# Kernel tuning notes

Hardware: AMD Instinct MI355X
Metric: run time of the kernel (lower is better)

## Reference

```python
import jax, jax.numpy as jnp
import numpy as np

N = 50000
IN_C = 128
OUT_C = 64


def gcn_conv(x, edge_index, W, b):
    # PyG GCNConv: h = X W; add self-loops; symmetric norm D^-1/2 (A+I) D^-1/2; aggregate; + bias
    n = x.shape[0]
    h = x @ W  # [N, out]
    loop = jnp.arange(n, dtype=edge_index.dtype)
    row = jnp.concatenate([edge_index[0], loop])  # source
    col = jnp.concatenate([edge_index[1], loop])  # target
    deg = jax.ops.segment_sum(jnp.ones_like(col, dtype=h.dtype), col, num_segments=n)
    dinv = jnp.where(deg > 0, jax.lax.rsqrt(deg), 0.0)
    norm = dinv[row] * dinv[col]  # [E+N]
    msg = norm[:, None] * h[row]  # gather source features
    out = jax.ops.segment_sum(msg, col, num_segments=n)  # scatter to targets
    return out + b


def layer_norm(x, w, b, eps=1e-5):
    mu = jnp.mean(x, axis=-1, keepdims=True)
    var = jnp.mean((x - mu) ** 2, axis=-1, keepdims=True)
    return (x - mu) * jax.lax.rsqrt(var + eps) * w + b


def setup_inputs() -> dict:
    key = jax.random.key(0)
    ks = jax.random.split(key, 10)
    x = jax.random.normal(ks[0], (N, IN_C), dtype=jnp.float32)
    edge_index = jax.random.randint(ks[1], (2, 800000), 0, N, dtype=jnp.int64)
    s1 = 1.0 / np.sqrt(IN_C)
    s2 = 1.0 / np.sqrt(OUT_C)
    W1 = jax.random.uniform(ks[2], (IN_C, OUT_C), jnp.float32, -s1, s1)
    b1 = jnp.zeros((OUT_C,), jnp.float32)
    ln_w = jnp.ones((OUT_C,), jnp.float32)
    ln_b = jnp.zeros((OUT_C,), jnp.float32)
    W2 = jax.random.uniform(ks[3], (OUT_C, OUT_C), jnp.float32, -s2, s2)
    b2 = jnp.zeros((OUT_C,), jnp.float32)
    W3 = jax.random.uniform(ks[4], (OUT_C, 6), jnp.float32, -s2, s2)
    b3 = jax.random.uniform(ks[5], (6,), jnp.float32, -s2, s2)
    return {"x": x, "edge_index": edge_index, "W1": W1, "b1": b1,
            "ln_w": ln_w, "ln_b": ln_b, "W2": W2, "b2": b2, "W3": W3, "b3": b3}


def reference(x, edge_index, W1, b1, ln_w, ln_b, W2, b2, W3, b3):
    h = gcn_conv(x, edge_index, W1, b1)           # [N, 64]
    h = jax.nn.relu(layer_norm(h, ln_w, ln_b))    # [N, 64]
    out1 = gcn_conv(h, edge_index, W2, b2)        # [N, 64]
    out2 = jax.nn.sigmoid(h @ W3 + b3)            # [N, 6]
    return (out1, out2)
```

## Files before the change

### kernel.cpp

```cpp
#include <hip/hip_runtime.h>
#include <hip/hip_fp16.h>
#include <math.h>


#define ELLW 48

typedef _Float16 half8 __attribute__((ext_vector_type(8)));
typedef float f32x4 __attribute__((ext_vector_type(4)));

__global__ void k_setup(const float* __restrict__ W1, const float* __restrict__ W2,
                        const float* __restrict__ W3, _Float16* __restrict__ W1g,
                        _Float16* __restrict__ Bg, int* __restrict__ cnt, int n) {
    if (blockIdx.x >= 52) {
        int i = (blockIdx.x - 52) * 256 + threadIdx.x;
        if (i < n) cnt[i] = 0;
        return;
    }
    int idx = blockIdx.x * 256 + threadIdx.x;
    if (idx < 8192) {
        int j = idx & 7, L = (idx >> 3) & 63, s = (idx >> 9) & 3, t = idx >> 11;
        int k = s * 32 + (L >> 4) * 8 + j;
        int c = t * 16 + (L & 15);
        W1g[idx] = (_Float16)W1[k * 64 + c];
    } else if (idx < 8192 + 5120) {
        int i2 = idx - 8192;
        int j = i2 & 7, L = (i2 >> 3) & 63, s = (i2 >> 9) & 1, u = i2 >> 10;
        int k = s * 32 + (L >> 4) * 8 + j;
        int c = (L & 15);
        float v;
        if (u < 4) v = W2[k * 64 + u * 16 + c];
        else v = (c < 6) ? W3[k * 6 + c] : 0.f;
        Bg[i2] = (_Float16)v;
    }
}

__global__ __launch_bounds__(256) void k_scatter(
    const int* __restrict__ row, const int* __restrict__ col,
    int* __restrict__ cnt, int* __restrict__ ell, int E, int slice_sz) {
    int slice = blockIdx.x & 7;
    int lo = slice * slice_sz;
    int hi = lo + slice_sz;
    int nchunk = gridDim.x >> 3;
    int stride = nchunk * 256;
    int v0 = (blockIdx.x >> 3) * 256 + threadIdx.x;
    int nv = E >> 2;
    const int4* c4p = (const int4*)col;
    const int4* r4p = (const int4*)row;
    for (int v = v0; v < nv; v += stride) {
        int4 c4 = c4p[v];
        int4 r4 = r4p[v];
        if (c4.x >= lo && c4.x < hi) {
            int rk = atomicAdd(&cnt[c4.x], 1);
            if (rk < ELLW) ell[c4.x * ELLW + rk] = r4.x << 7;
        }
        if (c4.y >= lo && c4.y < hi) {
            int rk = atomicAdd(&cnt[c4.y], 1);
            if (rk < ELLW) ell[c4.y * ELLW + rk] = r4.y << 7;
        }
        if (c4.z >= lo && c4.z < hi) {
            int rk = atomicAdd(&cnt[c4.z], 1);
            if (rk < ELLW) ell[c4.z * ELLW + rk] = r4.z << 7;
        }
        if (c4.w >= lo && c4.w < hi) {
            int rk = atomicAdd(&cnt[c4.w], 1);
            if (rk < ELLW) ell[c4.w * ELLW + rk] = r4.w << 7;
        }
    }
    if ((blockIdx.x >> 3) == 0) {
        for (int e = (nv << 2) + threadIdx.x; e < E; e += 256) {
            int c = col[e];
            if (c >= lo && c < hi) {
                int rk = atomicAdd(&cnt[c], 1);
                if (rk < ELLW) ell[c * ELLW + rk] = row[e] << 7;
            }
        }
    }
}

__global__ __launch_bounds__(256, 4) void k_gemm1(
    const float* __restrict__ x, const _Float16* __restrict__ W1g,
    const int* __restrict__ cnt, uint* __restrict__ hs,
    uint* __restrict__ h2s, int n) {
    int tid = threadIdx.x;
    if (blockIdx.x == 0) {
        if (tid < 32) hs[(size_t)n * 32 + tid] = 0u;
        else if (tid < 64) h2s[(size_t)n * 32 + (tid - 32)] = 0u;
    }
    int lane = tid & 63, wid = tid >> 6;
    int m16 = lane & 15, quad = lane >> 4;
    int node0 = blockIdx.x * 64 + wid * 16;
    int arow = node0 + m16;
    if (arow >= n) arow = n - 1;
    const float* xr = x + (size_t)arow * 128;
    half8 A[4];
#pragma unroll
    for (int s = 0; s < 4; s++) {
        const float4* p = (const float4*)(xr + s * 32 + quad * 8);
        float4 f0 = p[0], f1 = p[1];
        half8 a;
        a[0] = (_Float16)f0.x; a[1] = (_Float16)f0.y;
        a[2] = (_Float16)f0.z; a[3] = (_Float16)f0.w;
        a[4] = (_Float16)f1.x; a[5] = (_Float16)f1.y;
        a[6] = (_Float16)f1.z; a[7] = (_Float16)f1.w;
        A[s] = a;
    }
    float dsc[4];
#pragma unroll
    for (int r = 0; r < 4; r++) {
        int nd = node0 + quad * 4 + r;
        dsc[r] = rsqrtf((float)(cnt[nd < n ? nd : n - 1] + 1));
    }
    const half8* Wv = (const half8*)W1g;
#pragma unroll
    for (int t = 0; t < 4; t++) {
        f32x4 acc = {0.f, 0.f, 0.f, 0.f};
#pragma unroll
        for (int s = 0; s < 4; s++)
            acc = __builtin_amdgcn_mfma_f32_16x16x32_f16(A[s], Wv[(t * 4 + s) * 64 + lane], acc, 0, 0, 0);
#pragma unroll
        for (int r = 0; r < 4; r++) {
            int nd = node0 + quad * 4 + r;
            float v = acc[r] * dsc[r];
            float vo = __shfl_xor(v, 1, 64);
            if (!(m16 & 1) && nd < n) {
                __half2 pk = __floats2half2_rn(v, vo);
                hs[(size_t)nd * 32 + t * 8 + (m16 >> 1)] = *(uint*)&pk;
            }
        }
    }
}

#define GATHER_BODY8(SRC)                                                     \
    int2 o1[4], o2[4];                                                        \
    uint4 u0[4], u1[4];                                                       \
    {                                                                         \
        int2 o0[4];                                                           \
        _Pragma("unroll") for (int p = 0; p < 4; p++) o0[p] = ldidx2(p, 0);   \
        _Pragma("unroll") for (int p = 0; p < 4; p++) o1[p] = ldidx2(p, 8);   \
        _Pragma("unroll") for (int p = 0; p < 4; p++) {                       \
            uint2 t0 = *(const uint2*)(SRC + o0[p].x + m8);                   \
            uint2 t1 = *(const uint2*)(SRC + o0[p].y + m8);                   \
            u0[p].x = t0.x; u0[p].y = t0.y; u0[p].z = t1.x; u0[p].w = t1.y;   \
        }                                                                     \
    }                                                                         \
    for (int jb = 0; jb < Pmax; jb += 8) {                                    \
        _Pragma("unroll") for (int p = 0; p < 4; p++) o2[p] = ldidx2(p, jb + 16); \
        _Pragma("unroll") for (int p = 0; p < 4; p++) {                       \
            uint2 t0 = *(const uint2*)(SRC + o1[p].x + m8);                   \
            uint2 t1 = *(const uint2*)(SRC + o1[p].y + m8);                   \
            u1[p].x = t0.x; u1[p].y = t0.y; u1[p].z = t1.x; u1[p].w = t1.y;   \
        }                                                                     \
        _Pragma("unroll") for (int p = 0; p < 4; p++) {                       \
            float2 f;                                                         \
            f = __half22float2(*(__half2*)&u0[p].x); acc[p][0] += f.x; acc[p][1] += f.y; \
            f = __half22float2(*(__half2*)&u0[p].y); acc[p][2] += f.x; acc[p][3] += f.y; \
            f = __half22float2(*(__half2*)&u0[p].z); acc[p][0] += f.x; acc[p][1] += f.y; \
            f = __half22float2(*(__half2*)&u0[p].w); acc[p][2] += f.x; acc[p][3] += f.y; \
        }                                                                     \
        _Pragma("unroll") for (int p = 0; p < 4; p++) { o1[p] = o2[p]; u0[p] = u1[p]; } \
    }

#define GATHER_PROLOG(SRC_T)                                                  \
    int nid[4], st[4], P[4];                                                  \
    int Pmax = 0;                                                             \
    _Pragma("unroll") for (int p = 0; p < 4; p++) {                           \
        int node = base + wid * 4 + p;                                        \
        if (node >= n) node = n - 1;                                          \
        nid[p] = node;                                                        \
        st[p] = node * ELLW;                                                  \
        P[p] = cnt[node];                                                     \
        Pmax = Pmax > P[p] ? Pmax : P[p];                                     \
    }                                                                         \
    Pmax = (Pmax + 7) & ~7;                                                   \
    auto ldidx2 = [&](int p, int jb) -> int2 {                                \
        int2 o = *(const int2*)(ell + st[p] + jb + 2 * g);                    \
        int b = jb + 2 * g;                                                   \
        o.x = (b + 0 < P[p]) ? o.x : zoff;                                    \
        o.y = (b + 1 < P[p]) ? o.y : zoff;                                    \
        return o;                                                             \
    };                                                                        \
    const char* hsb = (const char*)(SRC_T);                                   \
    f32x4 acc[4];                                                             \
    _Pragma("unroll") for (int p = 0; p < 4; p++) {                           \
        int sa = (g == 0) ? (nid[p] << 7) : zoff;                             \
        uint2 us = *(const uint2*)(hsb + sa + m8);                            \
        float2 f0 = __half22float2(*(__half2*)&us.x);                         \
        float2 f1 = __half22float2(*(__half2*)&us.y);                         \
        acc[p][0] = f0.x; acc[p][1] = f0.y; acc[p][2] = f1.x; acc[p][3] = f1.y; \
    }

__global__ __launch_bounds__(256, 4) void k_conv1_fused(
    const uint* __restrict__ hs, const int* __restrict__ ell,
    const int* __restrict__ cnt, const float* __restrict__ b1,
    const float* __restrict__ lnw_g, const float* __restrict__ lnb_g,
    const _Float16* __restrict__ Bg, const float* __restrict__ b3,
    uint* __restrict__ h2s, float* __restrict__ out2, int zoff, int n) {
    __shared__ _Float16 Y[4][16 * 72];
    int tid = threadIdx.x;
    int lane = tid & 63, wid = tid >> 6;
    int m16l = lane & 15, g = lane >> 4;
    int m8 = m16l * 8;
    {
        float4 z = {0.f, 0.f, 0.f, 0.f};
        float4* yb = (float4*)Y[wid];
        for (int i = lane; i < 144; i += 64) yb[i] = z;
    }
    int base = blockIdx.x * 16;
    GATHER_PROLOG(hs)
    GATHER_BODY8(hsb)

    float4 b1v = ((const float4*)b1)[m16l];
    float4 lw = ((const float4*)lnw_g)[m16l];
    float4 lb = ((const float4*)lnb_g)[m16l];
    float dcs[4];
#pragma unroll
    for (int p = 0; p < 4; p++) {
        float s0 = acc[p][0], s1 = acc[p][1], s2 = acc[p][2], s3 = acc[p][3];
        s0 += __shfl_xor(s0, 16, 64); s0 += __shfl_xor(s0, 32, 64);
        s1 += __shfl_xor(s1, 16, 64); s1 += __shfl_xor(s1, 32, 64);
        s2 += __shfl_xor(s2, 16, 64); s2 += __shfl_xor(s2, 32, 64);
        s3 += __shfl_xor(s3, 16, 64); s3 += __shfl_xor(s3, 32, 64);
        float dc = rsqrtf((float)(P[p] + 1));
        dcs[p] = dc;
        float v0 = fmaf(dc, s0, b1v.x);
        float v1 = fmaf(dc, s1, b1v.y);
        float v2 = fmaf(dc, s2, b1v.z);
        float v3 = fmaf(dc, s3, b1v.w);
        float s = v0 + v1 + v2 + v3;
#pragma unroll
        for (int off = 8; off > 0; off >>= 1) s += __shfl_xor(s, off, 64);
        float mu = s * (1.f / 64.f);
        float d0 = v0 - mu, d1 = v1 - mu, d2 = v2 - mu, d3 = v3 - mu;
        float q = d0 * d0 + d1 * d1 + d2 * d2 + d3 * d3;
#pragma unroll
        for (int off = 8; off > 0; off >>= 1) q += __shfl_xor(q, off, 64);
        float rstd = rsqrtf(q * (1.f / 64.f) + 1e-5f);
        float y0 = fmaxf(fmaf(d0 * rstd, lw.x, lb.x), 0.f);
        float y1 = fmaxf(fmaf(d1 * rstd, lw.y, lb.y), 0.f);
        float y2 = fmaxf(fmaf(d2 * rstd, lw.z, lb.z), 0.f);
        float y3 = fmaxf(fmaf(d3 * rstd, lw.w, lb.w), 0.f);
        if (g == 0) {
            __half2 pk0 = __floats2half2_rn(y0, y1);
            __half2 pk1 = __floats2half2_rn(y2, y3);
            uint2 pk;
            pk.x = *(uint*)&pk0; pk.y = *(uint*)&pk1;
            *(uint2*)&Y[wid][p * 72 + 4 * m16l] = pk;
        }
    }
    int m16 = lane & 15, quad = lane >> 4;
    half8 a0 = *(const half8*)&Y[wid][m16 * 72 + quad * 8];
    half8 a1 = *(const half8*)&Y[wid][m16 * 72 + 32 + quad * 8];
    const half8* Bv = (const half8*)Bg;
    _Float16* h2h = (_Float16*)h2s;
#pragma unroll
    for (int t = 0; t < 4; t++) {
        f32x4 acc2 = {0.f, 0.f, 0.f, 0.f};
        acc2 = __builtin_amdgcn_mfma_f32_16x16x32_f16(a0, Bv[(t * 2 + 0) * 64 + lane], acc2, 0, 0, 0);
        acc2 = __builtin_amdgcn_mfma_f32_16x16x32_f16(a1, Bv[(t * 2 + 1) * 64 + lane], acc2, 0, 0, 0);
#pragma unroll
        for (int r = 0; r < 4; r++) {
            int nodep = base + wid * 4 + r;
            if (quad == 0 && nodep < n)
                h2h[(size_t)nodep * 64 + t * 16 + m16] = (_Float16)(acc2[r] * dcs[r]);
        }
    }
    {
        f32x4 acc2 = {0.f, 0.f, 0.f, 0.f};
        acc2 = __builtin_amdgcn_mfma_f32_16x16x32_f16(a0, Bv[8 * 64 + lane], acc2, 0, 0, 0);
        acc2 = __builtin_amdgcn_mfma_f32_16x16x32_f16(a1, Bv[9 * 64 + lane], acc2, 0, 0, 0);
        float bb = b3[m16 < 6 ? m16 : 0];
#pragma unroll
        for (int r = 0; r < 4; r++) {
            int nodep = base + wid * 4 + r;
            if (quad == 0 && m16 < 6 && nodep < n)
                out2[(size_t)nodep * 6 + m16] = 1.f / (1.f + __expf(-(acc2[r] + bb)));
        }
    }
}

__global__ __launch_bounds__(256, 4) void k_conv2(
    const uint* __restrict__ h2s, const int* __restrict__ ell,
    const int* __restrict__ cnt, const float* __restrict__ b2,
    float* __restrict__ out1, int zoff, int n) {
    int tid = threadIdx.x;
    int lane = tid & 63, wid = tid >> 6;
    int m16l = lane & 15, g = lane >> 4;
    int m8 = m16l * 8;
    int base = blockIdx.x * 16;
    GATHER_PROLOG(h2s)
    GATHER_BODY8(hsb)

    float4 b2v = ((const float4*)b2)[m16l];
#pragma unroll
    for (int p = 0; p < 4; p++) {
        float s0 = acc[p][0], s1 = acc[p][1], s2 = acc[p][2], s3 = acc[p][3];
        s0 += __shfl_xor(s0, 16, 64); s0 += __shfl_xor(s0, 32, 64);
        s1 += __shfl_xor(s1, 16, 64); s1 += __shfl_xor(s1, 32, 64);
        s2 += __shfl_xor(s2, 16, 64); s2 += __shfl_xor(s2, 32, 64);
        s3 += __shfl_xor(s3, 16, 64); s3 += __shfl_xor(s3, 32, 64);
        int node = base + wid * 4 + p;
        if (g == 0 && node < n) {
            float dc = rsqrtf((float)(P[p] + 1));
            float4 r;
            r.x = fmaf(dc, s0, b2v.x);
            r.y = fmaf(dc, s1, b2v.y);
            r.z = fmaf(dc, s2, b2v.z);
            r.w = fmaf(dc, s3, b2v.w);
            ((float4*)out1)[(size_t)node * 16 + m16l] = r;
        }
    }
}

extern "C" void kernel_launch(void* const* d_in, const int* in_sizes, int n_in,
                              void* d_out, int out_size, void* d_ws, size_t ws_size,
                              hipStream_t stream) {
    const float* x   = (const float*)d_in[0];
    const int*   ei  = (const int*)d_in[1];
    const float* W1  = (const float*)d_in[2];
    const float* b1  = (const float*)d_in[3];
    const float* lnw = (const float*)d_in[4];
    const float* lnb = (const float*)d_in[5];
    const float* W2  = (const float*)d_in[6];
    const float* b2  = (const float*)d_in[7];
    const float* W3  = (const float*)d_in[8];
    const float* b3  = (const float*)d_in[9];

    int n = in_sizes[0] / 128;
    int E = in_sizes[1] / 2;
    const int* row = ei;
    const int* col = ei + E;

    char* ws = (char*)d_ws;
    size_t off = 0;
    auto carve = [&](size_t bytes) -> char* {
        char* p = ws + off;
        off = (off + bytes + 255) & ~(size_t)255;
        return p;
    };
    int*   cnt  = (int*)carve(4 * (size_t)n);
    int*   ell  = (int*)carve(4 * ((size_t)n * ELLW + 256));
    uint*  hs   = (uint*)carve(128 * ((size_t)n + 1));
    uint*  h2s  = (uint*)carve(128 * ((size_t)n + 1));
    _Float16* W1g = (_Float16*)carve(2 * 8192);
    _Float16* Bg  = (_Float16*)carve(2 * 5120);

    float* out1 = (float*)d_out;
    float* out2 = out1 + (size_t)n * 64;
    int zero_off = n << 7;
    int slice_sz = (n + 7) / 8;

    k_setup<<<52 + (n + 255) / 256, 256, 0, stream>>>(W1, W2, W3, W1g, Bg, cnt, n);
    k_scatter<<<8 * 256, 256, 0, stream>>>(row, col, cnt, ell, E, slice_sz);
    k_gemm1<<<(n + 63) / 64, 256, 0, stream>>>(x, W1g, cnt, hs, h2s, n);
    k_conv1_fused<<<(n + 15) / 16, 256, 0, stream>>>(hs, ell, cnt,
                                                     b1, lnw, lnb, Bg, b3,
                                                     h2s, out2, zero_off, n);
    k_conv2<<<(n + 15) / 16, 256, 0, stream>>>(h2s, ell, cnt, b2,
                                               out1, zero_off, n);
}
```

Measured before the change: 187.6 us.

## Gather rows with 16-byte loads per lane and deepen the gather prefetch pipeline

The ELL gather in both convolution kernels now splits each 64-wide fp16 feature row across 8 lanes with 16-byte loads instead of 16 lanes with 8-byte loads. Each wave therefore works on 8 neighbours per node per step, one per lane group. The prefetch pipeline grows from one stage ahead to two, keeping more independent global loads in flight to hide gather latency. In exchange each lane holds 8 accumulators per node and more buffered uint4 registers, which can lower occupancy. The end-of-loop cross-lane reduction also grows from two shuffle steps to three per element.

New measurement: 192.8 us. 2.8% more time.

```diff
diff --git a/kernel.cpp b/kernel.cpp
--- a/kernel.cpp
+++ b/kernel.cpp
@@ -130,64 +130,73 @@
     }
 }
 
-#define GATHER_BODY8(SRC)                                                     \
-    int2 o1[4], o2[4];                                                        \
-    uint4 u0[4], u1[4];                                                       \
-    {                                                                         \
-        int2 o0[4];                                                           \
-        _Pragma("unroll") for (int p = 0; p < 4; p++) o0[p] = ldidx2(p, 0);   \
-        _Pragma("unroll") for (int p = 0; p < 4; p++) o1[p] = ldidx2(p, 8);   \
-        _Pragma("unroll") for (int p = 0; p < 4; p++) {                       \
-            uint2 t0 = *(const uint2*)(SRC + o0[p].x + m8);                   \
-            uint2 t1 = *(const uint2*)(SRC + o0[p].y + m8);                   \
-            u0[p].x = t0.x; u0[p].y = t0.y; u0[p].z = t1.x; u0[p].w = t1.y;   \
-        }                                                                     \
-    }                                                                         \
-    for (int jb = 0; jb < Pmax; jb += 8) {                                    \
-        _Pragma("unroll") for (int p = 0; p < 4; p++) o2[p] = ldidx2(p, jb + 16); \
-        _Pragma("unroll") for (int p = 0; p < 4; p++) {                       \
-            uint2 t0 = *(const uint2*)(SRC + o1[p].x + m8);                   \
-            uint2 t1 = *(const uint2*)(SRC + o1[p].y + m8);                   \
-            u1[p].x = t0.x; u1[p].y = t0.y; u1[p].z = t1.x; u1[p].w = t1.y;   \
-        }                                                                     \
-        _Pragma("unroll") for (int p = 0; p < 4; p++) {                       \
-            float2 f;                                                         \
-            f = __half22float2(*(__half2*)&u0[p].x); acc[p][0] += f.x; acc[p][1] += f.y; \
-            f = __half22float2(*(__half2*)&u0[p].y); acc[p][2] += f.x; acc[p][3] += f.y; \
-            f = __half22float2(*(__half2*)&u0[p].z); acc[p][0] += f.x; acc[p][1] += f.y; \
-            f = __half22float2(*(__half2*)&u0[p].w); acc[p][2] += f.x; acc[p][3] += f.y; \
-        }                                                                     \
-        _Pragma("unroll") for (int p = 0; p < 4; p++) { o1[p] = o2[p]; u0[p] = u1[p]; } \
-    }
-
 #define GATHER_PROLOG(SRC_T)                                                  \
-    int nid[4], st[4], P[4];                                                  \
+    int st[4], P[4], nid[4];                                                  \
     int Pmax = 0;                                                             \
     _Pragma("unroll") for (int p = 0; p < 4; p++) {                           \
         int node = base + wid * 4 + p;                                        \
         if (node >= n) node = n - 1;                                          \
-        nid[p] = node;                                                        \
-        st[p] = node * ELLW;                                                  \
-        P[p] = cnt[node];                                                     \
+        nid[p] = node; st[p] = node * ELLW; P[p] = cnt[node];                 \
         Pmax = Pmax > P[p] ? Pmax : P[p];                                     \
     }                                                                         \
     Pmax = (Pmax + 7) & ~7;                                                   \
-    auto ldidx2 = [&](int p, int jb) -> int2 {                                \
-        int2 o = *(const int2*)(ell + st[p] + jb + 2 * g);                    \
-        int b = jb + 2 * g;                                                   \
-        o.x = (b + 0 < P[p]) ? o.x : zoff;                                    \
-        o.y = (b + 1 < P[p]) ? o.y : zoff;                                    \
-        return o;                                                             \
+    auto ldix = [&](int p, int jb) -> int {                                   \
+        int o = ell[st[p] + jb + g];                                          \
+        return (jb + g < P[p]) ? o : zoff;                                    \
     };                                                                        \
     const char* hsb = (const char*)(SRC_T);                                   \
-    f32x4 acc[4];                                                             \
+    float accv[4][8];                                                         \
     _Pragma("unroll") for (int p = 0; p < 4; p++) {                           \
         int sa = (g == 0) ? (nid[p] << 7) : zoff;                             \
-        uint2 us = *(const uint2*)(hsb + sa + m8);                            \
-        float2 f0 = __half22float2(*(__half2*)&us.x);                         \
-        float2 f1 = __half22float2(*(__half2*)&us.y);                         \
-        acc[p][0] = f0.x; acc[p][1] = f0.y; acc[p][2] = f1.x; acc[p][3] = f1.y; \
-    }
+        uint4 us = *(const uint4*)(hsb + sa + m16b);                          \
+        float2 f;                                                             \
+        f = __half22float2(*(__half2*)&us.x); accv[p][0] = f.x; accv[p][1] = f.y; \
+        f = __half22float2(*(__half2*)&us.y); accv[p][2] = f.x; accv[p][3] = f.y; \
+        f = __half22float2(*(__half2*)&us.z); accv[p][4] = f.x; accv[p][5] = f.y; \
+        f = __half22float2(*(__half2*)&us.w); accv[p][6] = f.x; accv[p][7] = f.y; \
+    }
+
+#define CVT_ACC(p, U)                                                         \
+    {                                                                         \
+        float2 f;                                                             \
+        f = __half22float2(*(__half2*)&U.x); accv[p][0] += f.x; accv[p][1] += f.y; \
+        f = __half22float2(*(__half2*)&U.y); accv[p][2] += f.x; accv[p][3] += f.y; \
+        f = __half22float2(*(__half2*)&U.z); accv[p][4] += f.x; accv[p][5] += f.y; \
+        f = __half22float2(*(__half2*)&U.w); accv[p][6] += f.x; accv[p][7] += f.y; \
+    }
+
+#define GATHER_BODY16(SRC)                                                    \
+    {                                                                         \
+        int oC[4], oD[4];                                                     \
+        uint4 uA[4], uB[4], uC[4];                                            \
+        {                                                                     \
+            int oA[4], oB[4];                                                 \
+            _Pragma("unroll") for (int p = 0; p < 4; p++) oA[p] = ldix(p, 0); \
+            _Pragma("unroll") for (int p = 0; p < 4; p++) oB[p] = ldix(p, 8); \
+            _Pragma("unroll") for (int p = 0; p < 4; p++) oC[p] = ldix(p, 16);\
+            _Pragma("unroll") for (int p = 0; p < 4; p++)                     \
+                uA[p] = *(const uint4*)(SRC + oA[p] + m16b);                  \
+            _Pragma("unroll") for (int p = 0; p < 4; p++)                     \
+                uB[p] = *(const uint4*)(SRC + oB[p] + m16b);                  \
+        }                                                                     \
+        for (int jb = 0; jb < Pmax; jb += 8) {                                \
+            _Pragma("unroll") for (int p = 0; p < 4; p++) oD[p] = ldix(p, jb + 24); \
+            _Pragma("unroll") for (int p = 0; p < 4; p++)                     \
+                uC[p] = *(const uint4*)(SRC + oC[p] + m16b);                  \
+            _Pragma("unroll") for (int p = 0; p < 4; p++) CVT_ACC(p, uA[p])   \
+            _Pragma("unroll") for (int p = 0; p < 4; p++) {                   \
+                uA[p] = uB[p]; uB[p] = uC[p]; oC[p] = oD[p];                  \
+            }                                                                 \
+        }                                                                     \
+    }                                                                         \
+    _Pragma("unroll") for (int p = 0; p < 4; p++)                             \
+        _Pragma("unroll") for (int c = 0; c < 8; c++) {                       \
+            float v = accv[p][c];                                             \
+            v += __shfl_xor(v, 8, 64);                                        \
+            v += __shfl_xor(v, 16, 64);                                       \
+            v += __shfl_xor(v, 32, 64);                                       \
+            accv[p][c] = v;                                                   \
+        }
 
 __global__ __launch_bounds__(256, 4) void k_conv1_fused(
     const uint* __restrict__ hs, const int* __restrict__ ell,
@@ -198,8 +207,8 @@
     __shared__ _Float16 Y[4][16 * 72];
     int tid = threadIdx.x;
     int lane = tid & 63, wid = tid >> 6;
-    int m16l = lane & 15, g = lane >> 4;
-    int m8 = m16l * 8;
+    int l = lane & 7, g = lane >> 3;
+    int m16b = l * 16;
     {
         float4 z = {0.f, 0.f, 0.f, 0.f};
         float4* yb = (float4*)Y[wid];
@@ -207,44 +216,47 @@
     }
     int base = blockIdx.x * 16;
     GATHER_PROLOG(hs)
-    GATHER_BODY8(hsb)
-
-    float4 b1v = ((const float4*)b1)[m16l];
-    float4 lw = ((const float4*)lnw_g)[m16l];
-    float4 lb = ((const float4*)lnb_g)[m16l];
+    GATHER_BODY16(hsb)
+
+    float4 bvlo = ((const float4*)b1)[2 * l], bvhi = ((const float4*)b1)[2 * l + 1];
+    float4 lwlo = ((const float4*)lnw_g)[2 * l], lwhi = ((const float4*)lnw_g)[2 * l + 1];
+    float4 lblo = ((const float4*)lnb_g)[2 * l], lbhi = ((const float4*)lnb_g)[2 * l + 1];
     float dcs[4];
 #pragma unroll
     for (int p = 0; p < 4; p++) {
-        float s0 = acc[p][0], s1 = acc[p][1], s2 = acc[p][2], s3 = acc[p][3];
-        s0 += __shfl_xor(s0, 16, 64); s0 += __shfl_xor(s0, 32, 64);
-        s1 += __shfl_xor(s1, 16, 64); s1 += __shfl_xor(s1, 32, 64);
-        s2 += __shfl_xor(s2, 16, 64); s2 += __shfl_xor(s2, 32, 64);
-        s3 += __shfl_xor(s3, 16, 64); s3 += __shfl_xor(s3, 32, 64);
         float dc = rsqrtf((float)(P[p] + 1));
         dcs[p] = dc;
-        float v0 = fmaf(dc, s0, b1v.x);
-        float v1 = fmaf(dc, s1, b1v.y);
-        float v2 = fmaf(dc, s2, b1v.z);
-        float v3 = fmaf(dc, s3, b1v.w);
-        float s = v0 + v1 + v2 + v3;
-#pragma unroll
-        for (int off = 8; off > 0; off >>= 1) s += __shfl_xor(s, off, 64);
+        float v[8];
+        v[0] = fmaf(dc, accv[p][0], bvlo.x); v[1] = fmaf(dc, accv[p][1], bvlo.y);
+        v[2] = fmaf(dc, accv[p][2], bvlo.z); v[3] = fmaf(dc, accv[p][3], bvlo.w);
+        v[4] = fmaf(dc, accv[p][4], bvhi.x); v[5] = fmaf(dc, accv[p][5], bvhi.y);
+        v[6] = fmaf(dc, accv[p][6], bvhi.z); v[7] = fmaf(dc, accv[p][7], bvhi.w);
+        float s = ((v[0] + v[1]) + (v[2] + v[3])) + ((v[4] + v[5]) + (v[6] + v[7]));
+        s += __shfl_xor(s, 1, 64); s += __shfl_xor(s, 2, 64); s += __shfl_xor(s, 4, 64);
         float mu = s * (1.f / 64.f);
-        float d0 = v0 - mu, d1 = v1 - mu, d2 = v2 - mu, d3 = v3 - mu;
-        float q = d0 * d0 + d1 * d1 + d2 * d2 + d3 * d3;
-#pragma unroll
-        for (int off = 8; off > 0; off >>= 1) q += __shfl_xor(q, off, 64);
+        float d[8], q = 0.f;
+#pragma unroll
+        for (int c = 0; c < 8; c++) { d[c] = v[c] - mu; q += d[c] * d[c]; }
+        q += __shfl_xor(q, 1, 64); q += __shfl_xor(q, 2, 64); q += __shfl_xor(q, 4, 64);
         float rstd = rsqrtf(q * (1.f / 64.f) + 1e-5f);
-        float y0 = fmaxf(fmaf(d0 * rstd, lw.x, lb.x), 0.f);
-        float y1 = fmaxf(fmaf(d1 * rstd, lw.y, lb.y), 0.f);
-        float y2 = fmaxf(fmaf(d2 * rstd, lw.z, lb.z), 0.f);
-        float y3 = fmaxf(fmaf(d3 * rstd, lw.w, lb.w), 0.f);
+        float y[8];
+        y[0] = fmaxf(fmaf(d[0] * rstd, lwlo.x, lblo.x), 0.f);
+        y[1] = fmaxf(fmaf(d[1] * rstd, lwlo.y, lblo.y), 0.f);
+        y[2] = fmaxf(fmaf(d[2] * rstd, lwlo.z, lblo.z), 0.f);
+        y[3] = fmaxf(fmaf(d[3] * rstd, lwlo.w, lblo.w), 0.f);
+        y[4] = fmaxf(fmaf(d[4] * rstd, lwhi.x, lbhi.x), 0.f);
+        y[5] = fmaxf(fmaf(d[5] * rstd, lwhi.y, lbhi.y), 0.f);
+        y[6] = fmaxf(fmaf(d[6] * rstd, lwhi.z, lbhi.z), 0.f);
+        y[7] = fmaxf(fmaf(d[7] * rstd, lwhi.w, lbhi.w), 0.f);
         if (g == 0) {
-            __half2 pk0 = __floats2half2_rn(y0, y1);
-            __half2 pk1 = __floats2half2_rn(y2, y3);
-            uint2 pk;
+            __half2 pk0 = __floats2half2_rn(y[0], y[1]);
+            __half2 pk1 = __floats2half2_rn(y[2], y[3]);
+            __half2 pk2 = __floats2half2_rn(y[4], y[5]);
+            __half2 pk3 = __floats2half2_rn(y[6], y[7]);
+            uint4 pk;
             pk.x = *(uint*)&pk0; pk.y = *(uint*)&pk1;
-            *(uint2*)&Y[wid][p * 72 + 4 * m16l] = pk;
+            pk.z = *(uint*)&pk2; pk.w = *(uint*)&pk3;
+            *(uint4*)&Y[wid][p * 72 + 8 * l] = pk;
         }
     }
     int m16 = lane & 15, quad = lane >> 4;
@@ -284,29 +296,29 @@
     float* __restrict__ out1, int zoff, int n) {
     int tid = threadIdx.x;
     int lane = tid & 63, wid = tid >> 6;
-    int m16l = lane & 15, g = lane >> 4;
-    int m8 = m16l * 8;
+    int l = lane & 7, g = lane >> 3;
+    int m16b = l * 16;
     int base = blockIdx.x * 16;
     GATHER_PROLOG(h2s)
-    GATHER_BODY8(hsb)
-
-    float4 b2v = ((const float4*)b2)[m16l];
+    GATHER_BODY16(hsb)
+
+    float4 b2lo = ((const float4*)b2)[2 * l], b2hi = ((const float4*)b2)[2 * l + 1];
 #pragma unroll
     for (int p = 0; p < 4; p++) {
-        float s0 = acc[p][0], s1 = acc[p][1], s2 = acc[p][2], s3 = acc[p][3];
-        s0 += __shfl_xor(s0, 16, 64); s0 += __shfl_xor(s0, 32, 64);
-        s1 += __shfl_xor(s1, 16, 64); s1 += __shfl_xor(s1, 32, 64);
-        s2 += __shfl_xor(s2, 16, 64); s2 += __shfl_xor(s2, 32, 64);
-        s3 += __shfl_xor(s3, 16, 64); s3 += __shfl_xor(s3, 32, 64);
         int node = base + wid * 4 + p;
         if (g == 0 && node < n) {
             float dc = rsqrtf((float)(P[p] + 1));
-            float4 r;
-            r.x = fmaf(dc, s0, b2v.x);
-            r.y = fmaf(dc, s1, b2v.y);
-            r.z = fmaf(dc, s2, b2v.z);
-            r.w = fmaf(dc, s3, b2v.w);
-            ((float4*)out1)[(size_t)node * 16 + m16l] = r;
+            float4 r0, r1;
+            r0.x = fmaf(dc, accv[p][0], b2lo.x);
+            r0.y = fmaf(dc, accv[p][1], b2lo.y);
+            r0.z = fmaf(dc, accv[p][2], b2lo.z);
+            r0.w = fmaf(dc, accv[p][3], b2lo.w);
+            r1.x = fmaf(dc, accv[p][4], b2hi.x);
+            r1.y = fmaf(dc, accv[p][5], b2hi.y);
+            r1.z = fmaf(dc, accv[p][6], b2hi.z);
+            r1.w = fmaf(dc, accv[p][7], b2hi.w);
+            ((float4*)out1)[(size_t)node * 16 + 2 * l] = r0;
+            ((float4*)out1)[(size_t)node * 16 + 2 * l + 1] = r1;
         }
     }
 }
```
